# Kernel tuning notes

Measured on AMD Instinct MI355X. Metric: run time of the kernel, lower is better.

Reference implementation:

```python
import jax, jax.numpy as jnp
import numpy as np

EPS = 1e-8
LOG_EPS = 1e-20  # guard before log for categorical logits


def setup_inputs() -> dict:
    key = jax.random.key(0)
    B, T, K, I = 64, 1024, 512, 4
    k1, k2, k3, k4 = jax.random.split(key, 4)
    data = jax.random.randint(k1, (B, T), 0, K)
    masks = jax.random.bernoulli(k2, 0.5, (B, T)).astype(jnp.float32)
    init_p = jax.random.uniform(k3, (K,), dtype=jnp.float32)
    init_p = init_p / (init_p.sum() + EPS)
    P = jax.random.uniform(k4, (K, K), dtype=jnp.float32)
    P = P / (P.sum(axis=1, keepdims=True) + EPS)
    return {
        "data": data,
        "masks": masks,
        "init_probability": init_p,
        "transition_probability": P,
        "nb_imputation": I,
    }


def _forward_filter(data, masks, init_p, P):
    """HMM forward filtering. Returns messages [T, B, K]."""
    B, T = data.shape
    K = init_p.shape[0]
    oh = jax.nn.one_hot(data, K, dtype=init_p.dtype)      # [B,T,K]
    m = masks[..., None]                                   # [B,T,1]
    msg0 = init_p[None, :] * (1.0 - m[:, 0]) + m[:, 0] * oh[:, 0]
    msg0 = msg0 / (msg0.sum(-1, keepdims=True) + EPS)

    def step(prev, xs):
        oh_i, m_i = xs                                     # [B,K],[B,1]
        msg = (prev @ P) * (1.0 - m_i) + m_i * oh_i
        msg = msg / msg.sum(-1, keepdims=True)             # source uses no eps for t>=1
        return msg, msg

    xs = (jnp.moveaxis(oh[:, 1:], 1, 0), jnp.moveaxis(m[:, 1:], 1, 0))
    _, rest = jax.lax.scan(step, msg0, xs)                 # [T-1,B,K]
    return jnp.concatenate([msg0[None], rest], axis=0)    # [T,B,K]


def reference(data, masks, init_probability, transition_probability, nb_imputation):
    B, T = data.shape
    K = init_probability.shape[0]
    I = nb_imputation
    P = transition_probability

    messages = _forward_filter(data, masks, init_probability, P)  # [T,B,K]

    key = jax.random.key(42)
    k_last, k_seq = jax.random.split(key)

    # --- sample last timestep ---
    logp_last = jnp.log(messages[-1] + LOG_EPS)            # [B,K]
    s_last = jax.random.categorical(k_last, logp_last[:, None, :], shape=(B, I))
    m_last = masks[:, -1][:, None] > 0
    d_last = data[:, -1][:, None]
    # NOTE: faithful to source, last step uses mask*sample + (1-mask)*data
    out_last = jnp.where(m_last, s_last, d_last)           # [B,I]

    # --- backward sampling scan, t = T-2 .. 0 ---
    PT = P.T                                               # row j = P[:, j]
    keys = jax.random.split(k_seq, T - 1)

    def bstep(s_next, xs):
        msg_i, m_i, d_i, k_i = xs                          # [B,K],[B],[B],key
        trans = PT[s_next]                                 # [B,I,K] = P[:, s_next].T
        w = msg_i[:, None, :] * (trans + 1.0 / K)
        w = w / (w.sum(-1, keepdims=True) + EPS)
        s = jax.random.categorical(k_i, jnp.log(w + LOG_EPS))  # [B,I]
        # other steps: (1-mask)*sample + mask*data
        s = jnp.where(m_i[:, None] > 0, d_i[:, None], s)
        return s, s

    xs = (
        messages[: T - 1][::-1],                           # [T-1,B,K]
        masks[:, : T - 1].T[::-1],                         # [T-1,B]
        data[:, : T - 1].T[::-1],                          # [T-1,B]
        keys,
    )
    _, samples = jax.lax.scan(bstep, out_last, xs)         # [T-1,B,I] reversed time
    samples = samples[::-1]
    out = jnp.concatenate([samples, out_last[None]], axis=0)  # [T,B,I]
    return jnp.moveaxis(out, 0, 2)                         # [B,I,T]
```

## Files before the change

### kernel.cpp

```cpp
#include <hip/hip_runtime.h>
#include <stdint.h>


#define JAX_PARTITIONABLE 1

#define B_ 64
#define T_ 1024
#define K_ 512
#define I_ 4
#define NCHAIN (B_ * I_)
#define POWSLOT (513 * 512)
#define LMAX_WANT 8
#define MAXRUNS 32769
#define BWD_BLOCKS 8192
#define GEMM_BLOCKS (17 * 16)
#define SORT_BLOCKS 129

typedef double f64x4 __attribute__((ext_vector_type(4)));

__host__ __device__ inline void tf2x32(uint32_t k0, uint32_t k1, uint32_t c0, uint32_t c1,
                                       uint32_t& o0, uint32_t& o1) {
  uint32_t ks2 = k0 ^ k1 ^ 0x1BD11BDAu;
  uint32_t x0 = c0 + k0;
  uint32_t x1 = c1 + k1;
#define TFR(r) { x0 += x1; x1 = (x1 << (r)) | (x1 >> (32 - (r))); x1 ^= x0; }
  TFR(13) TFR(15) TFR(26) TFR(6)
  x0 += k1; x1 += ks2 + 1u;
  TFR(17) TFR(29) TFR(16) TFR(24)
  x0 += ks2; x1 += k0 + 2u;
  TFR(13) TFR(15) TFR(26) TFR(6)
  x0 += k0; x1 += k1 + 3u;
  TFR(17) TFR(29) TFR(16) TFR(24)
  x0 += k1; x1 += ks2 + 4u;
  TFR(13) TFR(15) TFR(26) TFR(6)
  x0 += ks2; x1 += k0 + 5u;
#undef TFR
  o0 = x0; o1 = x1;
}

__device__ inline uint32_t rng_bits(uint32_t kj0, uint32_t kj1, uint32_t e) {
#if JAX_PARTITIONABLE
  uint32_t a, b;
  tf2x32(kj0, kj1, 0u, e, a, b);
  return a ^ b;
#else
  const uint32_t HALF = (uint32_t)(NCHAIN * K_ / 2);
  uint32_t a, b;
  if (e < HALF) { tf2x32(kj0, kj1, e, e + HALF, a, b); return a; }
  else          { tf2x32(kj0, kj1, e - HALF, e, a, b); return b; }
#endif
}

__device__ inline float gumbel_scale(uint32_t bits) {
  float f = __uint_as_float((bits >> 9) | 0x3F800000u) - 1.0f;
  float u = f + 1.17549435e-38f;
  int iu = __float_as_int(u);
  float ef = (float)((iu >> 23) - 127);
  float m = __int_as_float((iu & 0x007fffff) | 0x3f800000);
  int big = m > 1.41421356f;
  m = big ? m * 0.5f : m;
  ef = big ? ef + 1.0f : ef;
  float fm = m - 1.0f;
  float r = fm * __builtin_amdgcn_rcpf(m + 1.0f);
  float r2 = r * r;
  float p = fmaf(r2, fmaf(r2, fmaf(r2, fmaf(r2, 0.11111111f, 0.14285715f),
                                   0.2f), 0.33333334f), 1.0f);
  float logu = fmaf(ef, 0.69314718f, (r + r) * p);
  return -__builtin_amdgcn_rcpf(logu);
}

__device__ inline void step_key(uint32_t ks0, uint32_t ks1, int j, uint32_t& kj0, uint32_t& kj1) {
#if JAX_PARTITIONABLE
  tf2x32(ks0, ks1, 0u, (uint32_t)j, kj0, kj1);
#else
  const int N = T_ - 1;
  uint32_t o0, o1;
  int v = 2 * j;
  if (v < N) { tf2x32(ks0, ks1, (uint32_t)v, (uint32_t)(v + N), o0, o1); kj0 = o0; }
  else       { tf2x32(ks0, ks1, (uint32_t)(v - N), (uint32_t)v, o0, o1); kj0 = o1; }
  v = 2 * j + 1;
  if (v < N) { tf2x32(ks0, ks1, (uint32_t)v, (uint32_t)(v + N), o0, o1); kj1 = o0; }
  else       { tf2x32(ks0, ks1, (uint32_t)(v - N), (uint32_t)v, o0, o1); kj1 = o1; }
#endif
}

__global__ __launch_bounds__(256) void setup_fused(
    const float* __restrict__ P, const float* __restrict__ initp,
    float* __restrict__ POW0, float* __restrict__ PTp,
    float* __restrict__ INITROW, float* __restrict__ V1,
    int* __restrict__ runCount, int* __restrict__ maxLdev, int* __restrict__ histcur,
    uint32_t* __restrict__ KEY0, uint32_t* __restrict__ KEY1,
    uint32_t ks0, uint32_t ks1) {
  int blk = blockIdx.x;
  if (blk < 1024) {
    int id = blk * 256 + threadIdx.x;
    int r = id >> 9, c = id & 511;
    float v = P[id];
    POW0[id] = v;
    PTp[c * 512 + r] = v + 0.001953125f;
    if (id < 512) INITROW[id] = initp[id];
    if (id < 128) histcur[id] = 0;
    if (id == 0) { *runCount = 0; *maxLdev = 1; }
  } else if (blk < 1026) {
    int c = (blk - 1024) * 256 + threadIdx.x;
    double acc = 0.0;
    for (int j = 0; j < 512; ++j) acc += (double)initp[j] * (double)P[j * 512 + c];
    V1[c] = (float)acc;
  } else {
    int j = (blk - 1026) * 256 + threadIdx.x;
    if (j < T_ - 1) {
      uint32_t a, b;
      step_key(ks0, ks1, j, a, b);
      KEY0[j] = a; KEY1[j] = b;
    }
  }
}

__global__ __launch_bounds__(1024) void setup_offsets_par(
    const int* __restrict__ data, const float* __restrict__ masks,
    int* __restrict__ off, int lmax, int initoff,
    int* __restrict__ runs, int* __restrict__ runCount, int* __restrict__ maxLdev,
    int* __restrict__ hist) {
  __shared__ int prevObs[1024];
  __shared__ int nextObs[1024];
  __shared__ int lhist[64];
  __shared__ int lmaxL;
  int b = blockIdx.x;
  int t = threadIdx.x;
  bool obs = masks[b * T_ + t] > 0.0f;
  prevObs[t] = obs ? t : -1;
  nextObs[t] = obs ? t : T_;
  if (t < 64) lhist[t] = 0;
  if (t == 0) lmaxL = 1;
  __syncthreads();
  for (int o = 1; o < 1024; o <<= 1) {
    int pv = (t >= o) ? prevObs[t - o] : -1;
    int nv = (t + o < 1024) ? nextObs[t + o] : T_;
    __syncthreads();
    if (pv > prevObs[t]) prevObs[t] = pv;
    if (nv < nextObs[t]) nextObs[t] = nv;
    __syncthreads();
  }
  int t0 = (t > 0) ? prevObs[t - 1] : -1;
  int idx = b * T_ + t;
  if (obs) off[idx] = -1;
  else if (t0 >= 0) {
    int L = t - t0; if (L > lmax) L = lmax;
    off[idx] = (L - 1) * POWSLOT + data[b * T_ + t0] * 512;
  } else if (t == 0) off[idx] = initoff;
  else {
    int L = t; if (L > lmax) L = lmax;
    off[idx] = (L - 1) * POWSLOT + 512 * 512;
  }
  if (!obs && t <= T_ - 2 && (t == 0 || masks[b * T_ + t - 1] > 0.0f)) {
    int te = nextObs[t] - 1; if (te > T_ - 2) te = T_ - 2;
    int r = atomicAdd(runCount, 1);
    if (r < MAXRUNS) {
      runs[r] = (b << 20) | (t << 10) | te;
      int steps = te - t + 1;
      int bkt = steps < 63 ? steps : 63;
      atomicAdd(&lhist[bkt], 1);
      int maxL = (t == 0) ? te : (te - t + 1);
      if (maxL > 1) atomicMax(&lmaxL, maxL);
    }
  }
  __syncthreads();
  if (t < 64) {
    int c = lhist[t];
    if (c) atomicAdd(&hist[t], c);
  }
  if (t == 0) {
    int v = lmaxL;
    if (v > 1) atomicMax(maxLdev, v);
  }
}

__global__ __launch_bounds__(256) void power_gemm_mfma(
    float* __restrict__ POW, int m, int lmax, const int* __restrict__ maxLdev,
    int sortN, const int* __restrict__ runs, const int* __restrict__ runCount,
    const int* __restrict__ hist, int* __restrict__ cursor,
    int* __restrict__ runsSorted) {
  if (blockIdx.x >= GEMM_BLOCKS) {
    if (sortN && blockIdx.y == 0) {
      __shared__ int lhist2[64];
      __shared__ int gbase[64];
      __shared__ int sbase[64];
      int tid = threadIdx.x;
      int i = (blockIdx.x - GEMM_BLOCKS) * 256 + tid;
      int total = *runCount; if (total > MAXRUNS) total = MAXRUNS;
      bool valid = i < total;
      if (tid < 64) lhist2[tid] = 0;
      __syncthreads();
      int r = 0, bkt = 0, lr = 0;
      if (valid) {
        r = runs[i];
        int ta = (r >> 10) & 1023, tb = r & 1023;
        int steps = tb - ta + 1;
        bkt = steps < 63 ? steps : 63;
        lr = atomicAdd(&lhist2[bkt], 1);
      }
      __syncthreads();
      if (tid < 64) {
        int c = lhist2[tid];
        gbase[tid] = c ? atomicAdd(&cursor[tid], c) : 0;
        int s = 0;
        for (int l = tid + 1; l < 64; ++l) s += hist[l];
        sbase[tid] = s;
      }
      __syncthreads();
      if (valid) runsSorted[sbase[bkt] + gbase[bkt] + lr] = r;
    }
    return;
  }
  int y = blockIdx.y;
  {
    int gate = *maxLdev; if (gate > lmax) gate = lmax;
    if (y + 1 + m > gate) return;
  }
  const float* A  = POW + (size_t)y * POWSLOT;
  const float* Bm = POW + (size_t)(m - 1) * POWSLOT;
  float* C        = POW + (size_t)(y + m) * POWSLOT;
  __shared__ double As[32][33];
  __shared__ double Bs[32][33];
  int tid = threadIdx.x;
  int lane = tid & 63;
  int wv = tid >> 6;
  int wr = wv >> 1, wc = wv & 1;
  int q = lane >> 4, r16 = lane & 15;
  int r0 = (blockIdx.x >> 4) * 32;
  int c0 = (blockIdx.x & 15) * 32;

  f64x4 z = {0.0, 0.0, 0.0, 0.0};
  f64x4 d1 = __builtin_amdgcn_mfma_f64_16x16x4f64((double)r16, 1.0, z, 0, 0, 0);
  f64x4 d2 = __builtin_amdgcn_mfma_f64_16x16x4f64(1.0, (double)r16, z, 0, 0, 0);
  int ir[4], ic[4];
#pragma unroll
  for (int v = 0; v < 4; ++v) {
    ir[v] = (((int)d1[v]) >> 2) & 15;
    ic[v] = (((int)d2[v]) >> 2) & 15;
  }

  int sr = tid >> 3;
  int sk4 = (tid & 7) * 4;
  int ar = r0 + sr; if (ar > 512) ar = 512;

  f64x4 acc = {0.0, 0.0, 0.0, 0.0};
  for (int kc = 0; kc < 512; kc += 32) {
    float4 av = *(const float4*)(A + (size_t)ar * 512 + kc + sk4);
    float4 bv = *(const float4*)(Bm + (size_t)(kc + sr) * 512 + c0 + sk4);
    __syncthreads();
    As[sk4 + 0][sr] = (double)av.x;
    As[sk4 + 1][sr] = (double)av.y;
    As[sk4 + 2][sr] = (double)av.z;
    As[sk4 + 3][sr] = (double)av.w;
    Bs[sr][sk4 + 0] = (double)bv.x;
    Bs[sr][sk4 + 1] = (double)bv.y;
    Bs[sr][sk4 + 2] = (double)bv.z;
    Bs[sr][sk4 + 3] = (double)bv.w;
    __syncthreads();
#pragma unroll
    for (int ks = 0; ks < 8; ++ks) {
      double a = As[ks * 4 + q][wr * 16 + r16];
      double b = Bs[ks * 4 + q][wc * 16 + r16];
      acc = __builtin_amdgcn_mfma_f64_16x16x4f64(a, b, acc, 0, 0, 0);
    }
  }
#pragma unroll
  for (int v = 0; v < 4; ++v) {
    int gr = r0 + wr * 16 + ir[v];
    int gc = c0 + wc * 16 + ic[v];
    if (gr < 513) C[(size_t)gr * 512 + gc] = (float)acc[v];
  }
}

__global__ __launch_bounds__(256) void backward_run(
    const int* __restrict__ data, const float* __restrict__ masks,
    const float* __restrict__ wsF, const int* __restrict__ off,
    const float* __restrict__ PTp,
    const uint32_t* __restrict__ KEY0, const uint32_t* __restrict__ KEY1,
    const int* __restrict__ runs, const int* __restrict__ runCount,
    int* __restrict__ out) {
  {
    int id = blockIdx.x * 256 + threadIdx.x;
    if (id < NCHAIN * T_) {
      int t = id & (T_ - 1);
      int b = id >> 12;
      if (t == T_ - 1 || masks[b * T_ + t] > 0.0f) out[id] = data[b * T_ + t];
    }
  }
  int lane = threadIdx.x & 63;
  int wv = threadIdx.x >> 6;
  int wid = blockIdx.x * 4 + wv;
  const int NW = BWD_BLOCKS * 4;
  int total = *runCount;
  if (total > MAXRUNS) total = MAXRUNS;
  total <<= 2;
  const float* wsL = wsF + (lane << 3);
  const float* ptL = PTp + (lane << 3);
  for (int u = wid; u < total; u += NW) {
    int run = runs[u >> 2];
    int ci = u & 3;
    int b = run >> 20, ta = (run >> 10) & 1023, tb = run & 1023;
    int s = data[b * T_ + tb + 1];
    uint32_t ebase = ((uint32_t)b << 11) | ((uint32_t)ci << 9) | ((uint32_t)(lane << 3));
    const int* offb = off + b * T_;
    int* outp = out + (((b << 2) | ci) * T_);
    for (int t = tb; t >= ta; --t) {
      int j = (T_ - 2) - t;
      uint32_t kj0 = KEY0[j], kj1 = KEY1[j];
      int o = offb[t];
      float4 m0 = *(const float4*)(wsL + o);
      float4 m1 = *(const float4*)(wsL + o + 4);
      const float* prow = ptL + ((size_t)s << 9);
      float4 p0 = *(const float4*)(prow);
      float4 p1 = *(const float4*)(prow + 4);
      float x0 = fmaf(m0.x, p0.x, 1e-20f) * gumbel_scale(rng_bits(kj0, kj1, ebase + 0u));
      float x1 = fmaf(m0.y, p0.y, 1e-20f) * gumbel_scale(rng_bits(kj0, kj1, ebase + 1u));
      float x2 = fmaf(m0.z, p0.z, 1e-20f) * gumbel_scale(rng_bits(kj0, kj1, ebase + 2u));
      float x3 = fmaf(m0.w, p0.w, 1e-20f) * gumbel_scale(rng_bits(kj0, kj1, ebase + 3u));
      float x4 = fmaf(m1.x, p1.x, 1e-20f) * gumbel_scale(rng_bits(kj0, kj1, ebase + 4u));
      float x5 = fmaf(m1.y, p1.y, 1e-20f) * gumbel_scale(rng_bits(kj0, kj1, ebase + 5u));
      float x6 = fmaf(m1.z, p1.z, 1e-20f) * gumbel_scale(rng_bits(kj0, kj1, ebase + 6u));
      float x7 = fmaf(m1.w, p1.w, 1e-20f) * gumbel_scale(rng_bits(kj0, kj1, ebase + 7u));
      float bv = x0; int bj = 0;
      if (x1 > bv) { bv = x1; bj = 1; }
      if (x2 > bv) { bv = x2; bj = 2; }
      if (x3 > bv) { bv = x3; bj = 3; }
      if (x4 > bv) { bv = x4; bj = 4; }
      if (x5 > bv) { bv = x5; bj = 5; }
      if (x6 > bv) { bv = x6; bj = 6; }
      if (x7 > bv) { bv = x7; bj = 7; }
      float wm = bv;
#pragma unroll
      for (int d = 1; d < 64; d <<= 1) wm = fmaxf(wm, __shfl_xor(wm, d));
      unsigned long long bal = __ballot(bv == wm);
      int wl = __ffsll(bal) - 1;
      int jw = __shfl(bj, wl);
      s = (wl << 3) + jw;
      if (lane == 0) outp[t] = s;
    }
  }
}

extern "C" void kernel_launch(void* const* d_in, const int* in_sizes, int n_in,
                              void* d_out, int out_size, void* d_ws, size_t ws_size,
                              hipStream_t stream) {
  const int* data = (const int*)d_in[0];
  const float* masks = (const float*)d_in[1];
  const float* initp = (const float*)d_in[2];
  const float* P = (const float*)d_in[3];
  int* out = (int*)d_out;

  int lmax = LMAX_WANT;
  {
    long long fixed = 512LL * 512 + 512 + (long long)B_ * T_ + 2 * (T_ - 1)
                      + 2LL * MAXRUNS + 256;
    long long avail = (long long)(ws_size / 4) - fixed;
    long long fit = avail / POWSLOT;
    if (fit < lmax) lmax = (fit < 1) ? 1 : (int)fit;
  }
  float* wsF = (float*)d_ws;
  float* POW = wsF;
  float* PTp = wsF + (size_t)lmax * POWSLOT;
  float* INITROW = PTp + 512 * 512;
  int* off = (int*)(INITROW + 512);
  uint32_t* KEY0 = (uint32_t*)(off + B_ * T_);
  uint32_t* KEY1 = KEY0 + (T_ - 1);
  int* runs = (int*)(KEY1 + (T_ - 1));
  int* runCount = runs + MAXRUNS;
  int* maxLdev = runCount + 1;
  int* histcur = runCount + 2;
  int* hist = histcur;
  int* cursor = histcur + 64;
  int* runsSorted = histcur + 128;
  int initoff = lmax * POWSLOT + 512 * 512;

  uint32_t ks0, ks1;
#if JAX_PARTITIONABLE
  tf2x32(0u, 42u, 0u, 1u, ks0, ks1);
#else
  {
    uint32_t a0, b0, a1, b1;
    tf2x32(0u, 42u, 0u, 2u, a0, b0);
    tf2x32(0u, 42u, 1u, 3u, a1, b1);
    ks0 = b0; ks1 = b1;
  }
#endif

  hipLaunchKernelGGL(setup_fused, dim3(1030), dim3(256), 0, stream,
                     P, initp, POW, PTp, INITROW, POW + 512 * 512,
                     runCount, maxLdev, histcur, KEY0, KEY1, ks0, ks1);
  hipLaunchKernelGGL(setup_offsets_par, dim3(B_), dim3(1024), 0, stream,
                     data, masks, off, lmax, initoff, runs, runCount, maxLdev, hist);
  int m = 1, first = 1;
  while (m < lmax) {
    int count = lmax - m; if (count > m) count = m;
    hipLaunchKernelGGL(power_gemm_mfma,
                       dim3(GEMM_BLOCKS + (first ? SORT_BLOCKS : 0), count), dim3(256), 0, stream,
                       POW, m, lmax, maxLdev,
                       first, runs, runCount, hist, cursor, runsSorted);
    first = 0;
    m += count;
  }
  if (first) {
    hipLaunchKernelGGL(power_gemm_mfma,
                       dim3(GEMM_BLOCKS + SORT_BLOCKS, 1), dim3(256), 0, stream,
                       POW, 1, lmax, maxLdev,
                       1, runs, runCount, hist, cursor, runsSorted);
  }
  hipLaunchKernelGGL(backward_run, dim3(BWD_BLOCKS), dim3(256), 0, stream,
                     data, masks, wsF, off, PTp, KEY0, KEY1, runsSorted, runCount, out);
}
```

Before: 322.8 us.

## Fuse setup kernels into one launch, prefetch GEMM tiles, lower power-table depth

Merges the two setup kernels into a single 130-block launch and replaces in-kernel counter initialisation with an async memset. The P copy and transpose now go through a shared-memory 64x64 tile, which should give coalesced writes. The init-vector product is split across two half-reductions. The power GEMM loads the next K-chunk into registers before computing the current one. The maximum matrix-power depth drops from 8 to 6, which shrinks the precompute but may shift more sequential work to the backward sampler. maxLdev now starts at 0 instead of 1.

```diff
diff --git a/kernel.cpp b/kernel.cpp
--- a/kernel.cpp
+++ b/kernel.cpp
@@ -10,7 +10,7 @@
 #define I_ 4
 #define NCHAIN (B_ * I_)
 #define POWSLOT (513 * 512)
-#define LMAX_WANT 8
+#define LMAX_WANT 6
 #define MAXRUNS 32769
 #define BWD_BLOCKS 8192
 #define GEMM_BLOCKS (17 * 16)
@@ -84,94 +84,107 @@
 #endif
 }
 
-__global__ __launch_bounds__(256) void setup_fused(
+__global__ __launch_bounds__(1024) void setup_all(
+    const int* __restrict__ data, const float* __restrict__ masks,
     const float* __restrict__ P, const float* __restrict__ initp,
     float* __restrict__ POW0, float* __restrict__ PTp,
     float* __restrict__ INITROW, float* __restrict__ V1,
-    int* __restrict__ runCount, int* __restrict__ maxLdev, int* __restrict__ histcur,
+    int* __restrict__ off, int lmax, int initoff,
+    int* __restrict__ runs, int* __restrict__ runCount, int* __restrict__ maxLdev,
+    int* __restrict__ hist,
     uint32_t* __restrict__ KEY0, uint32_t* __restrict__ KEY1,
     uint32_t ks0, uint32_t ks1) {
   int blk = blockIdx.x;
-  if (blk < 1024) {
-    int id = blk * 256 + threadIdx.x;
-    int r = id >> 9, c = id & 511;
-    float v = P[id];
-    POW0[id] = v;
-    PTp[c * 512 + r] = v + 0.001953125f;
-    if (id < 512) INITROW[id] = initp[id];
-    if (id < 128) histcur[id] = 0;
-    if (id == 0) { *runCount = 0; *maxLdev = 1; }
-  } else if (blk < 1026) {
-    int c = (blk - 1024) * 256 + threadIdx.x;
+  int tid = threadIdx.x;
+  if (blk < 64) {
+    __shared__ int prevObs[1024];
+    __shared__ int nextObs[1024];
+    __shared__ int lhist[64];
+    __shared__ int lmaxL;
+    int b = blk;
+    int t = tid;
+    bool obs = masks[b * T_ + t] > 0.0f;
+    prevObs[t] = obs ? t : -1;
+    nextObs[t] = obs ? t : T_;
+    if (t < 64) lhist[t] = 0;
+    if (t == 0) lmaxL = 1;
+    __syncthreads();
+    for (int o = 1; o < 1024; o <<= 1) {
+      int pv = (t >= o) ? prevObs[t - o] : -1;
+      int nv = (t + o < 1024) ? nextObs[t + o] : T_;
+      __syncthreads();
+      if (pv > prevObs[t]) prevObs[t] = pv;
+      if (nv < nextObs[t]) nextObs[t] = nv;
+      __syncthreads();
+    }
+    int t0 = (t > 0) ? prevObs[t - 1] : -1;
+    int idx = b * T_ + t;
+    if (obs) off[idx] = -1;
+    else if (t0 >= 0) {
+      int L = t - t0; if (L > lmax) L = lmax;
+      off[idx] = (L - 1) * POWSLOT + data[b * T_ + t0] * 512;
+    } else if (t == 0) off[idx] = initoff;
+    else {
+      int L = t; if (L > lmax) L = lmax;
+      off[idx] = (L - 1) * POWSLOT + 512 * 512;
+    }
+    if (!obs && t <= T_ - 2 && (t == 0 || masks[b * T_ + t - 1] > 0.0f)) {
+      int te = nextObs[t] - 1; if (te > T_ - 2) te = T_ - 2;
+      int r = atomicAdd(runCount, 1);
+      if (r < MAXRUNS) {
+        runs[r] = (b << 20) | (t << 10) | te;
+        int steps = te - t + 1;
+        int bkt = steps < 63 ? steps : 63;
+        atomicAdd(&lhist[bkt], 1);
+        int maxL = (t == 0) ? te : (te - t + 1);
+        if (maxL > 1) atomicMax(&lmaxL, maxL);
+      }
+    }
+    __syncthreads();
+    if (t < 64) {
+      int c = lhist[t];
+      if (c) atomicAdd(&hist[t], c);
+    }
+    if (t == 0) {
+      int v = lmaxL;
+      if (v > 1) atomicMax(maxLdev, v);
+    }
+  } else if (blk < 128) {
+    __shared__ float Tls[64][65];
+    int tt = blk - 64, tr = tt >> 3, tc = tt & 7;
+    int r = tid >> 4, c4 = (tid & 15) << 2;
+    int src = ((tr << 6) + r) * 512 + (tc << 6) + c4;
+    float4 v = *(const float4*)(P + src);
+    *(float4*)(POW0 + src) = v;
+    Tls[c4 + 0][r] = v.x;
+    Tls[c4 + 1][r] = v.y;
+    Tls[c4 + 2][r] = v.z;
+    Tls[c4 + 3][r] = v.w;
+    __syncthreads();
+    const float q = 0.001953125f;
+    float4 w;
+    w.x = Tls[r][c4 + 0] + q;
+    w.y = Tls[r][c4 + 1] + q;
+    w.z = Tls[r][c4 + 2] + q;
+    w.w = Tls[r][c4 + 3] + q;
+    *(float4*)(PTp + ((tc << 6) + r) * 512 + (tr << 6) + c4) = w;
+  } else if (blk == 128) {
+    __shared__ double vred[512];
+    int c = tid & 511, h = tid >> 9;
+    const float* Ph = P + h * 256 * 512;
+    const float* ih = initp + h * 256;
     double acc = 0.0;
-    for (int j = 0; j < 512; ++j) acc += (double)initp[j] * (double)P[j * 512 + c];
-    V1[c] = (float)acc;
+    for (int j = 0; j < 256; ++j) acc += (double)ih[j] * (double)Ph[j * 512 + c];
+    if (h == 0) vred[c] = acc;
+    __syncthreads();
+    if (h == 1) V1[c] = (float)(vred[c] + acc);
+    if (tid < 512) INITROW[tid] = initp[tid];
   } else {
-    int j = (blk - 1026) * 256 + threadIdx.x;
-    if (j < T_ - 1) {
+    if (tid < T_ - 1) {
       uint32_t a, b;
-      step_key(ks0, ks1, j, a, b);
-      KEY0[j] = a; KEY1[j] = b;
-    }
-  }
-}
-
-__global__ __launch_bounds__(1024) void setup_offsets_par(
-    const int* __restrict__ data, const float* __restrict__ masks,
-    int* __restrict__ off, int lmax, int initoff,
-    int* __restrict__ runs, int* __restrict__ runCount, int* __restrict__ maxLdev,
-    int* __restrict__ hist) {
-  __shared__ int prevObs[1024];
-  __shared__ int nextObs[1024];
-  __shared__ int lhist[64];
-  __shared__ int lmaxL;
-  int b = blockIdx.x;
-  int t = threadIdx.x;
-  bool obs = masks[b * T_ + t] > 0.0f;
-  prevObs[t] = obs ? t : -1;
-  nextObs[t] = obs ? t : T_;
-  if (t < 64) lhist[t] = 0;
-  if (t == 0) lmaxL = 1;
-  __syncthreads();
-  for (int o = 1; o < 1024; o <<= 1) {
-    int pv = (t >= o) ? prevObs[t - o] : -1;
-    int nv = (t + o < 1024) ? nextObs[t + o] : T_;
-    __syncthreads();
-    if (pv > prevObs[t]) prevObs[t] = pv;
-    if (nv < nextObs[t]) nextObs[t] = nv;
-    __syncthreads();
-  }
-  int t0 = (t > 0) ? prevObs[t - 1] : -1;
-  int idx = b * T_ + t;
-  if (obs) off[idx] = -1;
-  else if (t0 >= 0) {
-    int L = t - t0; if (L > lmax) L = lmax;
-    off[idx] = (L - 1) * POWSLOT + data[b * T_ + t0] * 512;
-  } else if (t == 0) off[idx] = initoff;
-  else {
-    int L = t; if (L > lmax) L = lmax;
-    off[idx] = (L - 1) * POWSLOT + 512 * 512;
-  }
-  if (!obs && t <= T_ - 2 && (t == 0 || masks[b * T_ + t - 1] > 0.0f)) {
-    int te = nextObs[t] - 1; if (te > T_ - 2) te = T_ - 2;
-    int r = atomicAdd(runCount, 1);
-    if (r < MAXRUNS) {
-      runs[r] = (b << 20) | (t << 10) | te;
-      int steps = te - t + 1;
-      int bkt = steps < 63 ? steps : 63;
-      atomicAdd(&lhist[bkt], 1);
-      int maxL = (t == 0) ? te : (te - t + 1);
-      if (maxL > 1) atomicMax(&lmaxL, maxL);
-    }
-  }
-  __syncthreads();
-  if (t < 64) {
-    int c = lhist[t];
-    if (c) atomicAdd(&hist[t], c);
-  }
-  if (t == 0) {
-    int v = lmaxL;
-    if (v > 1) atomicMax(maxLdev, v);
+      step_key(ks0, ks1, tid, a, b);
+      KEY0[tid] = a; KEY1[tid] = b;
+    }
   }
 }
 
@@ -245,9 +258,9 @@
   int ar = r0 + sr; if (ar > 512) ar = 512;
 
   f64x4 acc = {0.0, 0.0, 0.0, 0.0};
+  float4 av = *(const float4*)(A + (size_t)ar * 512 + sk4);
+  float4 bv = *(const float4*)(Bm + (size_t)sr * 512 + c0 + sk4);
   for (int kc = 0; kc < 512; kc += 32) {
-    float4 av = *(const float4*)(A + (size_t)ar * 512 + kc + sk4);
-    float4 bv = *(const float4*)(Bm + (size_t)(kc + sr) * 512 + c0 + sk4);
     __syncthreads();
     As[sk4 + 0][sr] = (double)av.x;
     As[sk4 + 1][sr] = (double)av.y;
@@ -257,6 +270,9 @@
     Bs[sr][sk4 + 1] = (double)bv.y;
     Bs[sr][sk4 + 2] = (double)bv.z;
     Bs[sr][sk4 + 3] = (double)bv.w;
+    int kn = (kc + 32 < 512) ? kc + 32 : 480;
+    av = *(const float4*)(A + (size_t)ar * 512 + kn + sk4);
+    bv = *(const float4*)(Bm + (size_t)(kn + sr) * 512 + c0 + sk4);
     __syncthreads();
 #pragma unroll
     for (int ks = 0; ks < 8; ++ks) {
@@ -387,11 +403,11 @@
   }
 #endif
 
-  hipLaunchKernelGGL(setup_fused, dim3(1030), dim3(256), 0, stream,
-                     P, initp, POW, PTp, INITROW, POW + 512 * 512,
-                     runCount, maxLdev, histcur, KEY0, KEY1, ks0, ks1);
-  hipLaunchKernelGGL(setup_offsets_par, dim3(B_), dim3(1024), 0, stream,
-                     data, masks, off, lmax, initoff, runs, runCount, maxLdev, hist);
+  hipMemsetAsync(runCount, 0, 130 * sizeof(int), stream);
+  hipLaunchKernelGGL(setup_all, dim3(130), dim3(1024), 0, stream,
+                     data, masks, P, initp, POW, PTp, INITROW, POW + 512 * 512,
+                     off, lmax, initoff, runs, runCount, maxLdev, hist,
+                     KEY0, KEY1, ks0, ks1);
   int m = 1, first = 1;
   while (m < lmax) {
     int count = lmax - m; if (count > m) count = m;
```

After: 299.7 us. 1.08x faster.
